# Performance work log

Measured on AMD Instinct MI355X. Metric: run time of the kernel, lower is better.

## Reference

```python
import jax, jax.numpy as jnp
import numpy as np

B, S, D, H = 4, 2048, 1024, 16
HD = D // H  # head_dim = 64


def setup_inputs() -> dict:
    key = jax.random.key(0)
    ks = jax.random.split(key, 5)
    scale = 1.0 / np.sqrt(D)
    return {
        "x": jax.random.normal(ks[0], (B, S, D), dtype=jnp.float32),
        "Wq": jax.random.normal(ks[1], (D, D), dtype=jnp.float32) * scale,
        "Wk": jax.random.normal(ks[2], (D, D), dtype=jnp.float32) * scale,
        "Wv": jax.random.normal(ks[3], (D, D), dtype=jnp.float32) * scale,
        "Wo": jax.random.normal(ks[4], (D, D), dtype=jnp.float32) * scale,
        "bo": jnp.zeros((D,), dtype=jnp.float32),
    }


def reference(x, Wq, Wk, Wv, Wo, bo):
    b, n, d_in = x.shape
    # projections: [b, n, d_out] -> [b, h, n, hd]
    def heads(t):
        return t.reshape(b, n, H, HD).transpose(0, 2, 1, 3)
    q = heads(x @ Wq)
    k = heads(x @ Wk)
    v = heads(x @ Wv)
    # attention scores [b, h, n, n], causal mask, scaled softmax
    scores = jnp.einsum('bhqd,bhkd->bhqk', q, k)
    causal = jnp.tril(jnp.ones((n, n), dtype=bool))  # True = keep
    scores = jnp.where(causal, scores, -jnp.inf)
    weights = jax.nn.softmax(scores / np.sqrt(HD), axis=-1)
    # context: [b, h, n, hd] -> [b, n, d_out]
    ctx = jnp.einsum('bhqk,bhkd->bhqd', weights, v)
    ctx = ctx.transpose(0, 2, 1, 3).reshape(b, n, D)
    return ctx @ Wo + bo
```

## Files before the change

### kernel.cpp

```cpp
#include <hip/hip_runtime.h>

#define B_ 4
#define S_ 2048
#define D_ 1024
#define H_ 16
#define HD_ 64

typedef __bf16 bf16x8 __attribute__((ext_vector_type(8)));
typedef float f32x4 __attribute__((ext_vector_type(4)));
typedef float f32x16 __attribute__((ext_vector_type(16)));
typedef unsigned short u16;
typedef unsigned short u16x8 __attribute__((ext_vector_type(8)));

__device__ __forceinline__ u16 f2b(float f) {
  unsigned u = __builtin_bit_cast(unsigned, f);
  return (u16)((u + 0x7FFFu + ((u >> 16) & 1u)) >> 16);
}

__device__ __forceinline__ void gll16(const void* g, void* l) {
  __builtin_amdgcn_global_load_lds(
      (const __attribute__((address_space(1))) void*)g,
      (__attribute__((address_space(3))) void*)l, 16, 0, 0);
}

__device__ __forceinline__ f32x4 mfma16(bf16x8 a, bf16x8 b, f32x4 c) {
  return __builtin_amdgcn_mfma_f32_16x16x32_bf16(a, b, c, 0, 0, 0);
}
__device__ __forceinline__ f32x16 mfma32(bf16x8 a, bf16x8 b, f32x16 c) {
  return __builtin_amdgcn_mfma_f32_32x32x16_bf16(a, b, c, 0, 0, 0);
}

__device__ __forceinline__ unsigned cvtpk(float lo, float hi) {
  unsigned r;
  asm("v_cvt_pk_bf16_f32 %0, %1, %2" : "=v"(r) : "v"(lo), "v"(hi));
  return r;
}
__device__ __forceinline__ void plswap(unsigned& a, unsigned& b) {
  asm("v_permlane32_swap_b32 %0, %1" : "+v"(a), "+v"(b));
}
__device__ __forceinline__ bf16x8 mk8(unsigned a, unsigned b, unsigned c, unsigned d) {
  union { unsigned u[4]; bf16x8 v; } x;
  x.u[0] = a; x.u[1] = b; x.u[2] = c; x.u[3] = d;
  return x.v;
}

__global__ __launch_bounds__(256) void k_cvt(const float* __restrict__ in,
                                             u16* __restrict__ out, int n4) {
  int i = blockIdx.x * 256 + threadIdx.x;
  if (i < n4) {
    float4 f = reinterpret_cast<const float4*>(in)[i];
    ushort4 o;
    o.x = f2b(f.x); o.y = f2b(f.y); o.z = f2b(f.z); o.w = f2b(f.w);
    reinterpret_cast<ushort4*>(out)[i] = o;
  }
}

__global__ __launch_bounds__(256) void k_wt4(
    const float* __restrict__ Wq, const float* __restrict__ Wk,
    const float* __restrict__ Wv, const float* __restrict__ Wo,
    u16* __restrict__ wqkvt, u16* __restrict__ wot) {
  __shared__ float tile[32][33];
  const float* W;
  u16* Wt;
  const int z = blockIdx.z;
  if (z == 0)      { W = Wq; Wt = wqkvt; }
  else if (z == 1) { W = Wk; Wt = wqkvt + (size_t)D_ * D_; }
  else if (z == 2) { W = Wv; Wt = wqkvt + (size_t)2 * D_ * D_; }
  else             { W = Wo; Wt = wot; }
  int bx = blockIdx.x * 32, by = blockIdx.y * 32;
  int tx = threadIdx.x, ty = threadIdx.y;
  #pragma unroll
  for (int i = ty; i < 32; i += 8)
    tile[i][tx] = W[(size_t)(by + i) * D_ + bx + tx];
  __syncthreads();
  #pragma unroll
  for (int i = ty; i < 32; i += 8)
    Wt[(size_t)(bx + i) * D_ + by + tx] = f2b(tile[tx][i]);
}

__global__ __launch_bounds__(512, 2) void k_gemm_qkv(
    const u16* __restrict__ A, const u16* __restrict__ Bt,
    u16* __restrict__ q, u16* __restrict__ kk, u16* __restrict__ v) {
  constexpr int K = D_;
  constexpr int NT = K / 64;
  __shared__ __align__(16) u16 lA[2 * 256 * 64];
  __shared__ __align__(16) u16 lB[2 * 256 * 64];
  const int cpx = 48;
  const int id = blockIdx.x;
  const int swz = (id & 7) * cpx + (id >> 3);
  const int bx = swz % 12, by = swz / 12;
  const int m0 = by * 256, n0 = bx * 256;
  const int t = threadIdx.x, lane = t & 63, w = t >> 6;
  const int wr = w >> 2, wc = w & 3;
  const int lr = lane & 15, lg = lane >> 4;
  const int l7 = lr & 7;
  const int wrlr = wr * 16 + lr, wclr = wc * 16 + lr;
  const int srow = t >> 3;
  const int sch = (t & 7) ^ (srow & 7);
  const u16* gAs = A + (size_t)(m0 + srow) * K + sch * 8;
  const u16* gBs = Bt + (size_t)(n0 + srow) * K + sch * 8;

  f32x4 acc[8][4] = {};
  bf16x8 Af[4][2], Bf0[2][2], Bf1[2][2];

  auto stageN = [&](int n) {
    if (n >= 4 * NT) return;
    const int kt2 = n >> 2, idx = n & 3;
    const int mat = idx & 1;
    const int h = (idx == 1 || idx == 2);
    const int bo = (kt2 & 1) * 16384;
    const u16* g = (mat ? gBs : gAs) + (size_t)(h * 128) * K + kt2 * 64;
    u16* l = (mat ? lB : lA) + bo + h * 8192 + t * 8;
    gll16(g, l);
    gll16(g + (size_t)64 * K, l + 4096);
  };

#define LOAD_A(qa_)                                                           \
  _Pragma("unroll") for (int il = 0; il < 4; ++il)                            \
  _Pragma("unroll") for (int ks = 0; ks < 2; ++ks)                            \
    Af[il][ks] = *(const bf16x8*)&lA[bufo + ((qa_)*128 + il * 32 + wrlr) * 64 +\
                                     (((ks * 4 + lg) ^ l7) * 8)];
#define LOAD_B(dst_, qb_)                                                     \
  _Pragma("unroll") for (int jl = 0; jl < 2; ++jl)                            \
  _Pragma("unroll") for (int ks = 0; ks < 2; ++ks)                            \
    dst_[jl][ks] = *(const bf16x8*)&lB[bufo + ((qb_)*128 + jl * 64 + wclr) * 64 +\
                                       (((ks * 4 + lg) ^ l7) * 8)];
#define MF(qa_, qb_, bf_)                                                     \
  __builtin_amdgcn_s_setprio(1);                                              \
  _Pragma("unroll") for (int il = 0; il < 4; ++il)                            \
  _Pragma("unroll") for (int jl = 0; jl < 2; ++jl)                            \
  _Pragma("unroll") for (int ks = 0; ks < 2; ++ks)                            \
    acc[(qa_)*4 + il][(qb_)*2 + jl] =                                         \
        mfma16(Af[il][ks], bf_[jl][ks], acc[(qa_)*4 + il][(qb_)*2 + jl]);     \
  __builtin_amdgcn_s_setprio(0);
#define BAR asm volatile("s_barrier" ::: "memory");
#define LGKM0 asm volatile("s_waitcnt lgkmcnt(0)" ::: "memory");

  for (int n = 0; n < 6; ++n) stageN(n);
  asm volatile("s_waitcnt vmcnt(4)" ::: "memory");
  BAR

  for (int kt = 0; kt < NT; ++kt) {
    const int bufo = (kt & 1) * 16384;
    const int nb = 4 * kt + 6;
    stageN(nb);
    LOAD_A(0) LOAD_B(Bf0, 0)
    BAR LGKM0
    MF(0, 0, Bf0)
    BAR
    stageN(nb + 1);
    LOAD_B(Bf1, 1)
    BAR LGKM0
    MF(0, 1, Bf1)
    BAR
    stageN(nb + 2);
    LOAD_A(1)
    BAR LGKM0
    MF(1, 1, Bf1)
    BAR
    stageN(nb + 3);
    if (kt < NT - 2) {
      asm volatile("s_waitcnt vmcnt(4)" ::: "memory");
    } else if (kt == NT - 2) {
      asm volatile("s_waitcnt vmcnt(0)" ::: "memory");
    }
    BAR
    MF(1, 0, Bf0)
    BAR
  }
#undef LOAD_A
#undef LOAD_B
#undef MF

  const int nclass = bx >> 2;
  const int b2 = m0 >> 11;
  const int s0b = m0 & 2047;
  const int h0 = (n0 & 1023) >> 6;
  if (nclass < 2) {
    u16* dst = nclass == 0 ? q : kk;
    const float sc = nclass == 0 ? 0.1803368801111f : 1.0f;
    #pragma unroll
    for (int i = 0; i < 8; ++i)
      #pragma unroll
      for (int j = 0; j < 4; ++j) {
        const size_t bh = (size_t)b2 * H_ + h0 + j;
        #pragma unroll
        for (int r = 0; r < 4; ++r) {
          int mloc = i * 32 + wr * 16 + lg * 4 + r;
          dst[(bh * S_ + s0b + mloc) * HD_ + wc * 16 + lr] =
              f2b(acc[i][j][r] * sc);
        }
      }
  } else {
    u16* vb = (u16*)lA;
    const int row = t >> 3, col0 = (t & 7) * 32;
    #pragma unroll
    for (int j = 0; j < 4; ++j) {
      __syncthreads();
      #pragma unroll
      for (int i = 0; i < 8; ++i)
        #pragma unroll
        for (int r = 0; r < 4; ++r)
          vb[(wc * 16 + lr) * 264 + i * 32 + wr * 16 + lg * 4 + r] =
              f2b(acc[i][j][r]);
      __syncthreads();
      u16* gv = v + ((size_t)(b2 * H_ + h0 + j) * HD_ + row) * S_ + s0b + col0;
      #pragma unroll
      for (int qq = 0; qq < 4; ++qq)
        *(u16x8*)(gv + qq * 8) = *(const u16x8*)&vb[row * 264 + col0 + qq * 8];
    }
  }
}

__global__ __launch_bounds__(512, 1) void k_gemm_proj2(
    const u16* __restrict__ A, const u16* __restrict__ Bt,
    const float* __restrict__ bias, float* __restrict__ out) {
  constexpr int K = D_;
  constexpr int NT = K / 64;
  __shared__ __align__(16) u16 lA[2 * 128 * 64];
  __shared__ __align__(16) u16 lB[2 * 256 * 64];
  const int cpx = 32;
  const int id = blockIdx.x;
  const int swz = (id & 7) * cpx + (id >> 3);
  const int bx = swz & 3, by = swz >> 2;
  const int m0 = by * 128, n0 = bx * 256;
  const int t = threadIdx.x, lane = t & 63, w = t >> 6;
  const int wr = w >> 2, wc = w & 3;
  const int lr = lane & 15, lg = lane >> 4;
  const int l7 = lr & 7;
  const int wrlr = wr * 16 + lr, wclr = wc * 16 + lr;
  const int srow = t >> 3;
  const int sch = (t & 7) ^ (srow & 7);
  const u16* gAs = A + (size_t)(m0 + srow) * K + sch * 8;
  const u16* gBs = Bt + (size_t)(n0 + srow) * K + sch * 8;

  f32x4 acc[4][4] = {};
  bf16x8 Af[2][2], Bf0[2][2], Bf1[2][2];

  auto stageN = [&](int n) {
    if (n >= 4 * NT) return;
    const int kt2 = n >> 2, idx = n & 3;
    const int koff = kt2 * 64;
    if (idx == 0) {
      gll16(gAs + koff, &lA[(kt2 & 1) * 8192 + t * 8]);
    } else if (idx == 2) {
      gll16(gAs + (size_t)64 * K + koff, &lA[(kt2 & 1) * 8192 + 4096 + t * 8]);
    } else if (idx == 1) {
      const u16* g = gBs + (size_t)128 * K + koff;
      u16* l = &lB[(kt2 & 1) * 16384 + 8192 + t * 8];
      gll16(g, l);
      gll16(g + (size_t)64 * K, l + 4096);
    } else {
      const u16* g = gBs + koff;
      u16* l = &lB[(kt2 & 1) * 16384 + t * 8];
      gll16(g, l);
      gll16(g + (size_t)64 * K, l + 4096);
    }
  };

#define LOAD_A(qa_)                                                           \
  _Pragma("unroll") for (int il = 0; il < 2; ++il)                            \
  _Pragma("unroll") for (int ks = 0; ks < 2; ++ks)                            \
    Af[il][ks] = *(const bf16x8*)&lA[bufoA + ((qa_)*64 + il * 32 + wrlr) * 64 +\
                                     (((ks * 4 + lg) ^ l7) * 8)];
#define LOAD_B(dst_, qb_)                                                     \
  _Pragma("unroll") for (int jl = 0; jl < 2; ++jl)                            \
  _Pragma("unroll") for (int ks = 0; ks < 2; ++ks)                            \
    dst_[jl][ks] = *(const bf16x8*)&lB[bufoB + ((qb_)*128 + jl * 64 + wclr) * 64 +\
                                       (((ks * 4 + lg) ^ l7) * 8)];
#define MF(qa_, qb_, bf_)                                                     \
  __builtin_amdgcn_s_setprio(1);                                              \
  _Pragma("unroll") for (int il = 0; il < 2; ++il)                            \
  _Pragma("unroll") for (int jl = 0; jl < 2; ++jl)                            \
  _Pragma("unroll") for (int ks = 0; ks < 2; ++ks)                            \
    acc[(qa_)*2 + il][(qb_)*2 + jl] =                                         \
        mfma16(Af[il][ks], bf_[jl][ks], acc[(qa_)*2 + il][(qb_)*2 + jl]);     \
  __builtin_amdgcn_s_setprio(0);

  for (int n = 0; n < 6; ++n) stageN(n);
  asm volatile("s_waitcnt vmcnt(3)" ::: "memory");
  BAR

  for (int kt = 0; kt < NT; ++kt) {
    const int bufoA = (kt & 1) * 8192;
    const int bufoB = (kt & 1) * 16384;
    const int nb = 4 * kt + 6;
    stageN(nb);
    LOAD_A(0) LOAD_B(Bf0, 0)
    BAR LGKM0
    MF(0, 0, Bf0)
    BAR
    stageN(nb + 1);
    LOAD_B(Bf1, 1)
    BAR LGKM0
    MF(0, 1, Bf1)
    BAR
    stageN(nb + 2);
    LOAD_A(1)
    BAR LGKM0
    MF(1, 1, Bf1)
    BAR
    stageN(nb + 3);
    if (kt < NT - 2) {
      asm volatile("s_waitcnt vmcnt(3)" ::: "memory");
    } else if (kt == NT - 2) {
      asm volatile("s_waitcnt vmcnt(0)" ::: "memory");
    }
    BAR
    MF(1, 0, Bf0)
    BAR
  }
#undef LOAD_A
#undef LOAD_B
#undef MF
#undef BAR
#undef LGKM0

  float bv[4];
  int nn[4];
  #pragma unroll
  for (int nj = 0; nj < 4; ++nj) {
    nn[nj] = n0 + (nj >> 1) * 128 + (nj & 1) * 64 + wc * 16 + lr;
    bv[nj] = bias[nn[nj]];
  }
  #pragma unroll
  for (int mi = 0; mi < 4; ++mi) {
    #pragma unroll
    for (int nj = 0; nj < 4; ++nj) {
      #pragma unroll
      for (int r = 0; r < 4; ++r) {
        int m = m0 + (mi >> 1) * 64 + (mi & 1) * 32 + wr * 16 + lg * 4 + r;
        out[(size_t)m * D_ + nn[nj]] = acc[mi][nj][r] + bv[nj];
      }
    }
  }
}

__global__ __launch_bounds__(256, 2) void k_attn(
    const u16* __restrict__ Qg, const u16* __restrict__ Kg,
    const u16* __restrict__ Vtg, u16* __restrict__ ctx) {
  __shared__ __align__(16) u16 Ks[2][64 * 64];
  __shared__ __align__(16) u16 Vs[2][64 * 64];
  const int ja = blockIdx.y, jb = 15 - ja, bh = blockIdx.x;
  const int t = threadIdx.x, l = t & 63, wq = t >> 6;
  const int lo5 = l & 31, hi = l >> 5, sw = l & 7;
  const size_t base = (size_t)bh * S_ * HD_;
  const int srow = t >> 3, sch = (t & 7) ^ (srow & 7);

  const int qw0A = ja * 128 + wq * 32, qw0B = jb * 128 + wq * 32;
  const int dktA = qw0A >> 6, dktB = qw0B >> 6;

  bf16x8 qA[4], qB[4];
  {
    const u16* qp = Qg + base + (size_t)(qw0A + lo5) * HD_ + hi * 8;
    #pragma unroll
    for (int di = 0; di < 4; ++di) qA[di] = *(const bf16x8*)(qp + di * 16);
    qp = Qg + base + (size_t)(qw0B + lo5) * HD_ + hi * 8;
    #pragma unroll
    for (int di = 0; di < 4; ++di) qB[di] = *(const bf16x8*)(qp + di * 16);
  }
  float mA = -1e30f, lsA = 0.f, mB = -1e30f, lsB = 0.f;
  f32x16 oA0 = {}, oA1 = {}, oB0 = {}, oB1 = {};

  auto stage = [&](int buf, int kb) {
    gll16(Kg + base + (size_t)(kb + srow) * HD_ + sch * 8, &Ks[buf][t * 8]);
    gll16(Kg + base + (size_t)(kb + 32 + srow) * HD_ + sch * 8, &Ks[buf][2048 + t * 8]);
    gll16(Vtg + base + (size_t)srow * S_ + kb + sch * 8, &Vs[buf][t * 8]);
    gll16(Vtg + base + (size_t)(32 + srow) * S_ + kb + sch * 8, &Vs[buf][2048 + t * 8]);
  };

  auto attend = [&](int buf, int kt, int qw0, int dkt, const bf16x8 (&qf)[4],
                    float& m_r, float& l_r, f32x16& o0, f32x16& o1) {
    const u16* KB = &Ks[buf][0];
    const u16* VB = &Vs[buf][0];
    f32x16 s0 = {}, s1 = {};
    #pragma unroll
    for (int di = 0; di < 4; ++di)
      s0 = mfma32(*(const bf16x8*)&KB[lo5 * 64 + (((di * 2 + hi) ^ sw) * 8)],
                  qf[di], s0);
    #pragma unroll
    for (int di = 0; di < 4; ++di)
      s1 = mfma32(*(const bf16x8*)&KB[(32 + lo5) * 64 + (((di * 2 + hi) ^ sw) * 8)],
                  qf[di], s1);
    if (kt == dkt) {
      int qrel = qw0 + lo5 - kt * 64;
      #pragma unroll
      for (int r = 0; r < 16; ++r) {
        int k0 = (r & 3) + 8 * (r >> 2) + 4 * hi;
        if (k0 > qrel) s0[r] = -1e30f;
        if (k0 + 32 > qrel) s1[r] = -1e30f;
      }
    }
    float tm = fmaxf(s0[0], s1[0]);
    #pragma unroll
    for (int r = 1; r < 16; ++r) tm = fmaxf(tm, fmaxf(s0[r], s1[r]));
    tm = fmaxf(tm, __shfl_xor(tm, 32));
    float mn = fmaxf(m_r, tm);
    float rescale = __builtin_amdgcn_exp2f(m_r - mn);
    m_r = mn;
    float sum = 0.f;
    #pragma unroll
    for (int r = 0; r < 16; ++r) { s0[r] = __builtin_amdgcn_exp2f(s0[r] - mn); sum += s0[r]; }
    #pragma unroll
    for (int r = 0; r < 16; ++r) { s1[r] = __builtin_amdgcn_exp2f(s1[r] - mn); sum += s1[r]; }
    sum += __shfl_xor(sum, 32);
    l_r = l_r * rescale + sum;
    o0 *= rescale;
    o1 *= rescale;
    unsigned a0 = cvtpk(s0[0], s0[1]), b0 = cvtpk(s0[4], s0[5]); plswap(a0, b0);
    unsigned a1 = cvtpk(s0[2], s0[3]), b1 = cvtpk(s0[6], s0[7]); plswap(a1, b1);
    unsigned a2 = cvtpk(s0[8], s0[9]), b2 = cvtpk(s0[12], s0[13]); plswap(a2, b2);
    unsigned a3 = cvtpk(s0[10], s0[11]), b3 = cvtpk(s0[14], s0[15]); plswap(a3, b3);
    bf16x8 p0 = mk8(a0, a1, b0, b1), p1 = mk8(a2, a3, b2, b3);
    a0 = cvtpk(s1[0], s1[1]); b0 = cvtpk(s1[4], s1[5]); plswap(a0, b0);
    a1 = cvtpk(s1[2], s1[3]); b1 = cvtpk(s1[6], s1[7]); plswap(a1, b1);
    a2 = cvtpk(s1[8], s1[9]); b2 = cvtpk(s1[12], s1[13]); plswap(a2, b2);
    a3 = cvtpk(s1[10], s1[11]); b3 = cvtpk(s1[14], s1[15]); plswap(a3, b3);
    bf16x8 p2 = mk8(a0, a1, b0, b1), p3 = mk8(a2, a3, b2, b3);
    o0 = mfma32(*(const bf16x8*)&VB[lo5 * 64 + (((0 + hi) ^ sw) * 8)], p0, o0);
    o0 = mfma32(*(const bf16x8*)&VB[lo5 * 64 + (((2 + hi) ^ sw) * 8)], p1, o0);
    o0 = mfma32(*(const bf16x8*)&VB[lo5 * 64 + (((4 + hi) ^ sw) * 8)], p2, o0);
    o0 = mfma32(*(const bf16x8*)&VB[lo5 * 64 + (((6 + hi) ^ sw) * 8)], p3, o0);
    o1 = mfma32(*(const bf16x8*)&VB[(32 + lo5) * 64 + (((0 + hi) ^ sw) * 8)], p0, o1);
    o1 = mfma32(*(const bf16x8*)&VB[(32 + lo5) * 64 + (((2 + hi) ^ sw) * 8)], p1, o1);
    o1 = mfma32(*(const bf16x8*)&VB[(32 + lo5) * 64 + (((4 + hi) ^ sw) * 8)], p2, o1);
    o1 = mfma32(*(const bf16x8*)&VB[(32 + lo5) * 64 + (((6 + hi) ^ sw) * 8)], p3, o1);
  };

  const int nt = 2 * jb + 2;
  stage(0, 0);
  __syncthreads();
  int cur = 0;
  for (int kt = 0; kt < nt; ++kt) {
    if (kt + 1 < nt) stage(cur ^ 1, (kt + 1) * 64);
    if (kt <= dktA) attend(cur, kt, qw0A, dktA, qA, mA, lsA, oA0, oA1);
    if (kt <= dktB) attend(cur, kt, qw0B, dktB, qB, mB, lsB, oB0, oB1);
    __syncthreads();
    cur ^= 1;
  }

  const int b = bh >> 4, h = bh & 15;
  {
    float inv = 1.f / lsA;
    u16* cp = ctx + ((size_t)b * S_ + qw0A + lo5) * D_ + h * 64 + hi * 4;
    #pragma unroll
    for (int rg = 0; rg < 4; ++rg) {
      ushort4 o4;
      o4.x = f2b(oA0[rg * 4 + 0] * inv); o4.y = f2b(oA0[rg * 4 + 1] * inv);
      o4.z = f2b(oA0[rg * 4 + 2] * inv); o4.w = f2b(oA0[rg * 4 + 3] * inv);
      *(ushort4*)(cp + rg * 8) = o4;
      o4.x = f2b(oA1[rg * 4 + 0] * inv); o4.y = f2b(oA1[rg * 4 + 1] * inv);
      o4.z = f2b(oA1[rg * 4 + 2] * inv); o4.w = f2b(oA1[rg * 4 + 3] * inv);
      *(ushort4*)(cp + 32 + rg * 8) = o4;
    }
  }
  {
    float inv = 1.f / lsB;
    u16* cp = ctx + ((size_t)b * S_ + qw0B + lo5) * D_ + h * 64 + hi * 4;
    #pragma unroll
    for (int rg = 0; rg < 4; ++rg) {
      ushort4 o4;
      o4.x = f2b(oB0[rg * 4 + 0] * inv); o4.y = f2b(oB0[rg * 4 + 1] * inv);
      o4.z = f2b(oB0[rg * 4 + 2] * inv); o4.w = f2b(oB0[rg * 4 + 3] * inv);
      *(ushort4*)(cp + rg * 8) = o4;
      o4.x = f2b(oB1[rg * 4 + 0] * inv); o4.y = f2b(oB1[rg * 4 + 1] * inv);
      o4.z = f2b(oB1[rg * 4 + 2] * inv); o4.w = f2b(oB1[rg * 4 + 3] * inv);
      *(ushort4*)(cp + 32 + rg * 8) = o4;
    }
  }
}

extern "C" void kernel_launch(void* const* d_in, const int* in_sizes, int n_in,
                              void* d_out, int out_size, void* d_ws, size_t ws_size,
                              hipStream_t stream) {
  const float* x  = (const float*)d_in[0];
  const float* Wq = (const float*)d_in[1];
  const float* Wk = (const float*)d_in[2];
  const float* Wv = (const float*)d_in[3];
  const float* Wo = (const float*)d_in[4];
  const float* bo = (const float*)d_in[5];
  float* out = (float*)d_out;
  (void)in_sizes; (void)n_in; (void)out_size; (void)ws_size;

  char* p = (char*)d_ws;
  const size_t NTOK = (size_t)B_ * S_;
  u16* xb    = (u16*)p; p += NTOK * D_ * 2;
  u16* wqkvt = (u16*)p; p += (size_t)3 * D_ * D_ * 2;
  u16* wot   = (u16*)p; p += (size_t)D_ * D_ * 2;
  u16* Qg    = (u16*)p; p += NTOK * D_ * 2;
  u16* Kg    = (u16*)p; p += NTOK * D_ * 2;
  u16* Vtg   = (u16*)p; p += NTOK * D_ * 2;
  u16* ctx   = (u16*)p; p += NTOK * D_ * 2;

  int n4 = (int)(NTOK * D_ / 4);
  k_cvt<<<dim3((n4 + 255) / 256), dim3(256), 0, stream>>>(x, xb, n4);
  k_wt4<<<dim3(32, 32, 4), dim3(32, 8), 0, stream>>>(Wq, Wk, Wv, Wo, wqkvt, wot);
  k_gemm_qkv<<<dim3(384), dim3(512), 0, stream>>>(xb, wqkvt, Qg, Kg, Vtg);
  k_attn<<<dim3(B_ * H_, 8), dim3(256), 0, stream>>>(Qg, Kg, Vtg, ctx);
  k_gemm_proj2<<<dim3(256), dim3(512), 0, stream>>>(ctx, wot, bo, out);
}
```

Baseline: 196.1 us.

## Restructure GEMM main loop into two phases with fewer barriers

Both projection GEMM main loops move from four barrier-separated quarter-steps per k-tile to two half-steps. Each half loads the A quarter plus both B quarters, then issues two MFMA groups back to back. The global-to-LDS stage issue order and the vmcnt wait thresholds are reordered to match. The goal is fewer s_barrier and lgkmcnt stalls per tile and longer uninterrupted MFMA runs. The cost is more registers for holding fragments, plus some risk in the staging and wait-count correctness, since it relies on which stage slots correspond to which buffer.

```diff
diff --git a/kernel.cpp b/kernel.cpp
--- a/kernel.cpp
+++ b/kernel.cpp
@@ -136,36 +136,29 @@
 #define BAR asm volatile("s_barrier" ::: "memory");
 #define LGKM0 asm volatile("s_waitcnt lgkmcnt(0)" ::: "memory");
 
-  for (int n = 0; n < 6; ++n) stageN(n);
-  asm volatile("s_waitcnt vmcnt(4)" ::: "memory");
-  BAR
+  stageN(0); stageN(1); stageN(3);
+  stageN(2);
+  stageN(4); stageN(5); stageN(7);
 
   for (int kt = 0; kt < NT; ++kt) {
     const int bufo = (kt & 1) * 16384;
-    const int nb = 4 * kt + 6;
-    stageN(nb);
-    LOAD_A(0) LOAD_B(Bf0, 0)
-    BAR LGKM0
-    MF(0, 0, Bf0)
-    BAR
-    stageN(nb + 1);
-    LOAD_B(Bf1, 1)
-    BAR LGKM0
-    MF(0, 1, Bf1)
-    BAR
-    stageN(nb + 2);
+    stageN(4 * (kt + 1) + 2);
+    if (kt < NT - 1) {
+      asm volatile("s_waitcnt vmcnt(8)" ::: "memory");
+    } else {
+      asm volatile("s_waitcnt vmcnt(0)" ::: "memory");
+    }
+    BAR
+    LOAD_A(0) LOAD_B(Bf0, 0) LOAD_B(Bf1, 1)
+    LGKM0
+    MF(0, 0, Bf0) MF(0, 1, Bf1)
+    BAR
+    stageN(4 * (kt + 2) + 0);
+    stageN(4 * (kt + 2) + 1);
+    stageN(4 * (kt + 2) + 3);
     LOAD_A(1)
-    BAR LGKM0
-    MF(1, 1, Bf1)
-    BAR
-    stageN(nb + 3);
-    if (kt < NT - 2) {
-      asm volatile("s_waitcnt vmcnt(4)" ::: "memory");
-    } else if (kt == NT - 2) {
-      asm volatile("s_waitcnt vmcnt(0)" ::: "memory");
-    }
-    BAR
-    MF(1, 0, Bf0)
+    LGKM0
+    MF(1, 0, Bf0) MF(1, 1, Bf1)
     BAR
   }
 #undef LOAD_A
@@ -277,37 +270,30 @@
         mfma16(Af[il][ks], bf_[jl][ks], acc[(qa_)*2 + il][(qb_)*2 + jl]);     \
   __builtin_amdgcn_s_setprio(0);
 
-  for (int n = 0; n < 6; ++n) stageN(n);
-  asm volatile("s_waitcnt vmcnt(3)" ::: "memory");
-  BAR
+  stageN(0); stageN(1); stageN(3);
+  stageN(2);
+  stageN(4); stageN(5); stageN(7);
 
   for (int kt = 0; kt < NT; ++kt) {
     const int bufoA = (kt & 1) * 8192;
     const int bufoB = (kt & 1) * 16384;
-    const int nb = 4 * kt + 6;
-    stageN(nb);
-    LOAD_A(0) LOAD_B(Bf0, 0)
-    BAR LGKM0
-    MF(0, 0, Bf0)
-    BAR
-    stageN(nb + 1);
-    LOAD_B(Bf1, 1)
-    BAR LGKM0
-    MF(0, 1, Bf1)
-    BAR
-    stageN(nb + 2);
+    stageN(4 * (kt + 1) + 2);
+    if (kt < NT - 1) {
+      asm volatile("s_waitcnt vmcnt(6)" ::: "memory");
+    } else {
+      asm volatile("s_waitcnt vmcnt(0)" ::: "memory");
+    }
+    BAR
+    LOAD_A(0) LOAD_B(Bf0, 0) LOAD_B(Bf1, 1)
+    LGKM0
+    MF(0, 0, Bf0) MF(0, 1, Bf1)
+    BAR
+    stageN(4 * (kt + 2) + 0);
+    stageN(4 * (kt + 2) + 1);
+    stageN(4 * (kt + 2) + 3);
     LOAD_A(1)
-    BAR LGKM0
-    MF(1, 1, Bf1)
-    BAR
-    stageN(nb + 3);
-    if (kt < NT - 2) {
-      asm volatile("s_waitcnt vmcnt(3)" ::: "memory");
-    } else if (kt == NT - 2) {
-      asm volatile("s_waitcnt vmcnt(0)" ::: "memory");
-    }
-    BAR
-    MF(1, 0, Bf0)
+    LGKM0
+    MF(1, 0, Bf0) MF(1, 1, Bf1)
     BAR
   }
 #undef LOAD_A
```

Result: faster. 178.4 us (-9.0%).
